# Optimization experiments

Hardware: AMD Instinct MI355X
Metric: run time of the kernel (lower is better)

Reference implementation:

```python
import jax, jax.numpy as jnp
import numpy as np

DIM = 512
LEVELS = 4
KSIZES = [3, 5, 7, 9]
NUM_HEADS = 4
GN_GROUPS = 4
GN_EPS = 1e-5
ROPE_BASE = 10000.0


def dwconv(x, w, b):
    # x: (B,C,H,W), w: (C,1,k,k) depthwise, b: (C,)
    y = jax.lax.conv_general_dilated(
        x, w, window_strides=(1, 1), padding='SAME',
        dimension_numbers=('NCHW', 'OIHW', 'NCHW'),
        feature_group_count=x.shape[1])
    return y + b[None, :, None, None]


def groupnorm(x, w, b):
    B, C, H, W = x.shape
    xg = x.reshape(B, GN_GROUPS, C // GN_GROUPS, H, W)
    mu = xg.mean(axis=(2, 3, 4), keepdims=True)
    var = xg.var(axis=(2, 3, 4), keepdims=True)
    xn = ((xg - mu) * jax.lax.rsqrt(var + GN_EPS)).reshape(B, C, H, W)
    return xn * w[None, :, None, None] + b[None, :, None, None]


def rope2d(x):
    # Faithful to the torch RoPE: rotations have shape (h, c//2) and broadcast
    # onto the trailing (w, c//2) dims of x (valid because h == w), so the
    # rotation angle effectively varies along the w axis.
    b, h, w, c = x.shape
    k_max = c // 2
    theta = 1.0 / (ROPE_BASE ** (jnp.arange(k_max, dtype=x.dtype) / k_max))
    angles = jnp.arange(h, dtype=x.dtype)[:, None] * theta[None, :]  # (h, k_max)
    cos = jnp.cos(angles)[None, None, :, :]  # broadcasts along w axis
    sin = jnp.sin(angles)[None, None, :, :]
    xp = x.reshape(b, h, w, k_max, 2)
    re, im = xp[..., 0], xp[..., 1]
    out_re = cos * re - sin * im
    out_im = cos * im + sin * re
    return jnp.stack([out_re, out_im], axis=-1).reshape(b, h, w, c)


def setup_inputs() -> dict:
    key = jax.random.key(0)
    ks = jax.random.split(key, 20)
    C = DIM
    inp = {'x': jax.random.normal(ks[0], (8, C, 64, 64), dtype=jnp.float32)}
    for i, k in enumerate(KSIZES):
        inp[f'conv_w{i}'] = jax.random.normal(ks[1 + i], (C, 1, k, k), dtype=jnp.float32) * 0.05
        inp[f'conv_b{i}'] = jnp.zeros((C,), dtype=jnp.float32)
        inp[f'gn_w{i}'] = jnp.ones((C,), dtype=jnp.float32)
        inp[f'gn_b{i}'] = jnp.zeros((C,), dtype=jnp.float32)
    inp['qk_w'] = jax.random.normal(ks[10], (2 * C, C), dtype=jnp.float32) * (C ** -0.5)
    inp['lepe_w'] = jax.random.normal(ks[11], (C, 1, 3, 3), dtype=jnp.float32) * 0.05
    inp['lepe_b'] = jnp.zeros((C,), dtype=jnp.float32)
    return inp


def reference(x, conv_w0, conv_b0, gn_w0, gn_b0, conv_w1, conv_b1, gn_w1, gn_b1,
              conv_w2, conv_b2, gn_w2, gn_b2, conv_w3, conv_b3, gn_w3, gn_b3,
              qk_w, lepe_w, lepe_b):
    conv_ws = [conv_w0, conv_w1, conv_w2, conv_w3]
    conv_bs = [conv_b0, conv_b1, conv_b2, conv_b3]
    gn_ws = [gn_w0, gn_w1, gn_w2, gn_w3]
    gn_bs = [gn_b0, gn_b1, gn_b2, gn_b3]

    # Multi-level depthwise conv -> GroupNorm -> sigmoid gate, averaged.
    fused = sum(jax.nn.sigmoid(groupnorm(dwconv(x, cw, cb), gw, gb))
                for cw, cb, gw, gb in zip(conv_ws, conv_bs, gn_ws, gn_bs)) / LEVELS

    b, c, h, w = fused.shape
    n = h * w
    H = NUM_HEADS
    hd = c // H

    tokens = fused.transpose(0, 2, 3, 1).reshape(b, n, c)  # (b, n, c)

    qk = tokens @ qk_w.T  # (b, n, 2c)
    q = jax.nn.elu(qk[..., :c]) + 1.0
    k = jax.nn.elu(qk[..., c:]) + 1.0
    v = tokens

    q_rope = rope2d(q.reshape(b, h, w, c)).reshape(b, n, H, hd).transpose(0, 2, 1, 3)
    k_rope = rope2d(k.reshape(b, h, w, c)).reshape(b, n, H, hd).transpose(0, 2, 1, 3)
    qh = q.reshape(b, n, H, hd).transpose(0, 2, 1, 3)  # (b,H,n,hd)
    kh = k.reshape(b, n, H, hd).transpose(0, 2, 1, 3)
    vh = v.reshape(b, n, H, hd).transpose(0, 2, 1, 3)

    k_mean = kh.mean(axis=2, keepdims=True)  # (b,H,1,hd)
    z = 1.0 / (jnp.einsum('bhnd,bhmd->bhnm', qh, k_mean) + 1e-6)  # (b,H,n,1)
    kv = jnp.einsum('bhnd,bhne->bhde', k_rope, vh) / n  # (b,H,hd,hd)
    attn = jnp.einsum('bhnd,bhde->bhne', q_rope, kv) * z  # (b,H,n,hd)

    out_tok = attn.transpose(0, 2, 1, 3).reshape(b, n, c)
    lepe_out = dwconv(fused, lepe_w, lepe_b)  # (b,c,h,w)
    out_tok = out_tok + lepe_out.transpose(0, 2, 3, 1).reshape(b, n, c)

    return out_tok.transpose(0, 2, 1).reshape(b, c, h, w)
```

## Files before the change

### kernel.cpp

```cpp
#include <hip/hip_runtime.h>
#include <math.h>


typedef __attribute__((ext_vector_type(8))) short bf8;
typedef __attribute__((ext_vector_type(4))) float f32x4;

__device__ __forceinline__ float waveSum(float v) {
  #pragma unroll
  for (int o = 32; o; o >>= 1) v += __shfl_down(v, o, 64);
  return v;
}

__device__ __forceinline__ unsigned short f2bf(float f) {
  unsigned u = __float_as_uint(f);
  unsigned r = u + 0x7fffu + ((u >> 16) & 1u);
  return (unsigned short)(r >> 16);
}

__device__ __forceinline__ float bf2f(unsigned short u) {
  return __uint_as_float((unsigned)u << 16);
}

__device__ __forceinline__ void gload_lds16(const void* g, void* l) {
  __builtin_amdgcn_global_load_lds(
      (const __attribute__((address_space(1))) unsigned*)g,
      (__attribute__((address_space(3))) unsigned*)l, 16, 0, 0);
}

__global__ __launch_bounds__(256) void k_ropetab(float* __restrict__ tab) {
  int idx = blockIdx.x * 256 + threadIdx.x;
  int w = idx >> 8, kk = idx & 255;
  float theta = powf(10000.0f, -(float)kk * (1.0f / 256.0f));
  float ang = (float)w * theta;
  tab[2 * idx]     = cosf(ang);
  tab[2 * idx + 1] = sinf(ang);
}

template <int K>
__device__ __forceinline__ void conv8(const float (*sm)[76], const float* wl,
                                      int r, int cb, float bias, float acc[8]) {
  constexpr int P = (K - 1) / 2;
  #pragma unroll
  for (int i = 0; i < 8; i++) acc[i] = bias;
  #pragma unroll
  for (int dy = 0; dy < K; ++dy) {
    const float* row = &sm[r + dy - P + 4][cb];
    float v[16];
    #pragma unroll
    for (int o = 0; o < 16; o += 4)
      *(float4*)&v[o] = *(const float4*)&row[o];
    #pragma unroll
    for (int dx = 0; dx < K; ++dx) {
      float wv = wl[dy * K + dx];
      #pragma unroll
      for (int i = 0; i < 8; i++)
        acc[i] = fmaf(wv, v[4 + i + dx - P], acc[i]);
    }
  }
}

__device__ __forceinline__ void load_plane512(const float* __restrict__ xp,
                                              float (*sm)[76], int tid) {
  for (int idx = tid; idx < 5184; idx += 512) {
    int pr = idx / 72, pc = idx - pr * 72;
    int gr = pr - 4, gc = pc - 4;
    float v = 0.f;
    if ((unsigned)gr < 64u && (unsigned)gc < 64u) v = xp[gr * 64 + gc];
    sm[pr][pc] = v;
  }
}

__device__ __forceinline__ void load_weights512(const float* w0, const float* w1,
                                                const float* w2, const float* w3,
                                                float* wl, int c, int tid) {
  if (tid < 9)               wl[tid] = w0[c * 9  + tid];
  else if (tid < 34)         wl[tid] = w1[c * 25 + tid - 9];
  else if (tid < 83)         wl[tid] = w2[c * 49 + tid - 34];
  else if (tid < 164)        wl[tid] = w3[c * 81 + tid - 83];
}

__device__ __forceinline__ void reduce_write2_512(float s, float sq, float* red,
                                                  int tid, float* dst) {
  s = waveSum(s); sq = waveSum(sq);
  int wid = tid >> 6, lane = tid & 63;
  if (lane == 0) { red[wid] = s; red[8 + wid] = sq; }
  __syncthreads();
  if (tid == 0) {
    float S = 0.f, SQ = 0.f;
    #pragma unroll
    for (int i = 0; i < 8; i++) { S += red[i]; SQ += red[8 + i]; }
    dst[0] = S; dst[1] = SQ;
  }
  __syncthreads();
}

__global__ __launch_bounds__(512) void k_conv4(
    const float* __restrict__ x,
    const float* __restrict__ w0, const float* __restrict__ b0,
    const float* __restrict__ w1, const float* __restrict__ b1,
    const float* __restrict__ w2, const float* __restrict__ b2,
    const float* __restrict__ w3, const float* __restrict__ b3,
    float* __restrict__ part,
    unsigned short* __restrict__ l0, unsigned short* __restrict__ l1,
    unsigned short* __restrict__ l2, unsigned short* __restrict__ l3) {
  __shared__ float sm[72][76];
  __shared__ float wl[164];
  __shared__ float red[16];
  int tid = threadIdx.x;
  int bc = blockIdx.x;
  int b = bc >> 9, c = bc & 511;
  load_plane512(x + (size_t)bc * 4096, sm, tid);
  load_weights512(w0, w1, w2, w3, wl, c, tid);
  __syncthreads();
  int r = tid >> 3, cb = (tid & 7) << 3;
  size_t obase = (size_t)bc * 4096 + r * 64 + cb;
  float acc[8];
  float s, sq;
  unsigned short o[8];

  conv8<3>(sm, &wl[0], r, cb, b0[c], acc);
  s = 0; sq = 0;
  #pragma unroll
  for (int i = 0; i < 8; i++) {
    s += acc[i]; sq = fmaf(acc[i], acc[i], sq); o[i] = f2bf(acc[i]);
  }
  *(uint4*)&l0[obase] = *(uint4*)&o[0];
  reduce_write2_512(s, sq, red, tid, part + ((size_t)(0 * 8 + b) * 512 + c) * 2);
  __builtin_amdgcn_sched_barrier(0);

  conv8<5>(sm, &wl[9], r, cb, b1[c], acc);
  s = 0; sq = 0;
  #pragma unroll
  for (int i = 0; i < 8; i++) {
    s += acc[i]; sq = fmaf(acc[i], acc[i], sq); o[i] = f2bf(acc[i]);
  }
  *(uint4*)&l1[obase] = *(uint4*)&o[0];
  reduce_write2_512(s, sq, red, tid, part + ((size_t)(1 * 8 + b) * 512 + c) * 2);
  __builtin_amdgcn_sched_barrier(0);

  conv8<7>(sm, &wl[34], r, cb, b2[c], acc);
  s = 0; sq = 0;
  #pragma unroll
  for (int i = 0; i < 8; i++) {
    s += acc[i]; sq = fmaf(acc[i], acc[i], sq); o[i] = f2bf(acc[i]);
  }
  *(uint4*)&l2[obase] = *(uint4*)&o[0];
  reduce_write2_512(s, sq, red, tid, part + ((size_t)(2 * 8 + b) * 512 + c) * 2);
  __builtin_amdgcn_sched_barrier(0);

  conv8<9>(sm, &wl[83], r, cb, b3[c], acc);
  s = 0; sq = 0;
  #pragma unroll
  for (int i = 0; i < 8; i++) {
    s += acc[i]; sq = fmaf(acc[i], acc[i], sq); o[i] = f2bf(acc[i]);
  }
  *(uint4*)&l3[obase] = *(uint4*)&o[0];
  reduce_write2_512(s, sq, red, tid, part + ((size_t)(3 * 8 + b) * 512 + c) * 2);
}

__global__ __launch_bounds__(128) void k_gn_stats(const float* __restrict__ part,
                                                  float* __restrict__ stats) {
  int blk = blockIdx.x;
  int tid = threadIdx.x;
  int g = blk & 3, bb = (blk >> 2) & 7, l = blk >> 5;
  const float* p = part + ((size_t)(l * 8 + bb) * 512 + g * 128 + tid) * 2;
  float s = p[0], sq = p[1];
  s = waveSum(s); sq = waveSum(sq);
  __shared__ float red[4];
  int wid = tid >> 6, lane = tid & 63;
  if (lane == 0) { red[wid] = s; red[2 + wid] = sq; }
  __syncthreads();
  if (tid == 0) {
    float S = red[0] + red[1], SQ = red[2] + red[3];
    const float inv = 1.0f / (128.0f * 4096.0f);
    float mean = S * inv;
    float var = SQ * inv - mean * mean;
    stats[blk * 2] = mean;
    stats[blk * 2 + 1] = rsqrtf(var + 1e-5f);
  }
}

__global__ __launch_bounds__(256) void k_fused_tp(
    const unsigned short* __restrict__ l0, const unsigned short* __restrict__ l1,
    const unsigned short* __restrict__ l2, const unsigned short* __restrict__ l3,
    const float* __restrict__ gw0, const float* __restrict__ gb0,
    const float* __restrict__ gw1, const float* __restrict__ gb1,
    const float* __restrict__ gw2, const float* __restrict__ gb2,
    const float* __restrict__ gw3, const float* __restrict__ gb3,
    const float* __restrict__ stats, float* __restrict__ fused,
    unsigned short* __restrict__ fbf) {
  __shared__ float smT[64][65];
  int tid = threadIdx.x;
  int bid = blockIdx.x;
  int nt = bid & 63, ct = (bid >> 6) & 7, b = bid >> 9;
  int c0 = ct << 6, n0 = nt << 6;
  int c_loc = tid >> 2, nq = tid & 3;
  int c = c0 + c_loc, g = c >> 7;
  float m0 = stats[(0 * 32 + b * 4 + g) * 2], r0 = stats[(0 * 32 + b * 4 + g) * 2 + 1];
  float m1 = stats[(1 * 32 + b * 4 + g) * 2], r1 = stats[(1 * 32 + b * 4 + g) * 2 + 1];
  float m2 = stats[(2 * 32 + b * 4 + g) * 2], r2 = stats[(2 * 32 + b * 4 + g) * 2 + 1];
  float m3 = stats[(3 * 32 + b * 4 + g) * 2], r3 = stats[(3 * 32 + b * 4 + g) * 2 + 1];
  float a0 = r0 * gw0[c], c0p = gb0[c] - m0 * a0;
  float a1 = r1 * gw1[c], c1p = gb1[c] - m1 * a1;
  float a2 = r2 * gw2[c], c2p = gb2[c] - m2 * a2;
  float a3 = r3 * gw3[c], c3p = gb3[c] - m3 * a3;
  size_t base = ((size_t)b * 512 + c) * 4096 + n0 + nq * 16;
  uint4 u0a = *(const uint4*)&l0[base], u0b = *(const uint4*)&l0[base + 8];
  uint4 u1a = *(const uint4*)&l1[base], u1b = *(const uint4*)&l1[base + 8];
  uint4 u2a = *(const uint4*)&l2[base], u2b = *(const uint4*)&l2[base + 8];
  uint4 u3a = *(const uint4*)&l3[base], u3b = *(const uint4*)&l3[base + 8];
  float outv[16];
  #pragma unroll
  for (int i = 0; i < 8; i++) {
    float t0 = fmaf(bf2f(((const unsigned short*)&u0a)[i]), a0, c0p);
    float t1 = fmaf(bf2f(((const unsigned short*)&u1a)[i]), a1, c1p);
    float t2 = fmaf(bf2f(((const unsigned short*)&u2a)[i]), a2, c2p);
    float t3 = fmaf(bf2f(((const unsigned short*)&u3a)[i]), a3, c3p);
    float s = 1.0f / (1.0f + __expf(-t0)) + 1.0f / (1.0f + __expf(-t1)) +
              1.0f / (1.0f + __expf(-t2)) + 1.0f / (1.0f + __expf(-t3));
    outv[i] = s * 0.25f;
  }
  #pragma unroll
  for (int i = 0; i < 8; i++) {
    float t0 = fmaf(bf2f(((const unsigned short*)&u0b)[i]), a0, c0p);
    float t1 = fmaf(bf2f(((const unsigned short*)&u1b)[i]), a1, c1p);
    float t2 = fmaf(bf2f(((const unsigned short*)&u2b)[i]), a2, c2p);
    float t3 = fmaf(bf2f(((const unsigned short*)&u3b)[i]), a3, c3p);
    float s = 1.0f / (1.0f + __expf(-t0)) + 1.0f / (1.0f + __expf(-t1)) +
              1.0f / (1.0f + __expf(-t2)) + 1.0f / (1.0f + __expf(-t3));
    outv[8 + i] = s * 0.25f;
  }
  float* fp = fused + base;
  #pragma unroll
  for (int i = 0; i < 16; i += 4)
    *(float4*)&fp[i] = make_float4(outv[i], outv[i + 1], outv[i + 2], outv[i + 3]);
  #pragma unroll
  for (int i = 0; i < 16; i++) smT[c_loc][nq * 16 + i] = outv[i];
  __syncthreads();
  int cc = tid & 63, r_s = tid >> 6;
  #pragma unroll
  for (int rr = 0; rr < 64; rr += 4)
    fbf[((size_t)b * 4096 + n0 + rr + r_s) * 512 + c0 + cc] = f2bf(smT[cc][rr + r_s]);
}

__global__ __launch_bounds__(256) void k_wcvt(const float* __restrict__ qkw,
                                              unsigned short* __restrict__ wbf) {
  int gid = blockIdx.x * 256 + threadIdx.x;
  float4 v = *(const float4*)&qkw[(size_t)gid * 4];
  short4 o;
  o.x = (short)f2bf(v.x); o.y = (short)f2bf(v.y);
  o.z = (short)f2bf(v.z); o.w = (short)f2bf(v.w);
  *(short4*)&wbf[(size_t)gid * 4] = o;
}

__global__ __launch_bounds__(256) void k_qk(const unsigned short* __restrict__ fbf,
                                            const unsigned short* __restrict__ wbf,
                                            float* __restrict__ qbuf,
                                            float* __restrict__ kbuf) {
  __shared__ __align__(16) short As[8192];
  __shared__ __align__(16) short Bs[8192];
  int tid = threadIdx.x;
  int bid = blockIdx.x;
  int sw = (bid & 7) * 256 + (bid >> 3);
  int b = sw >> 8, rem = sw & 255;
  int mt_blk = rem >> 3, jt = rem & 7;
  int m0 = mt_blk << 7, j0 = jt << 7;
  int lane = tid & 63, wid = tid >> 6;
  int wm = (wid >> 1) * 64, wn = (wid & 1) * 64;
  int l15 = lane & 15, l4 = lane >> 4;

  const unsigned short* Ab = fbf + (size_t)b * 4096 * 512;
  f32x4 acc[4][4];
  #pragma unroll
  for (int i = 0; i < 4; i++)
    #pragma unroll
    for (int j = 0; j < 4; j++) acc[i][j] = (f32x4)0.f;

  int srow[4], sperm[4];
  #pragma unroll
  for (int i = 0; i < 4; i++) {
    int s = i * 256 + tid;
    srow[i] = s >> 3;
    sperm[i] = (s & 7) ^ (srow[i] & 7);
  }

  for (int t = 0; t < 8; ++t) {
    int c0 = t << 6;
    if (t) __syncthreads();
    #pragma unroll
    for (int i = 0; i < 4; i++) {
      int s = i * 256 + tid;
      gload_lds16(Ab + (size_t)(m0 + srow[i]) * 512 + c0 + sperm[i] * 8,
                  (char*)As + s * 16);
      gload_lds16(wbf + (size_t)(j0 + srow[i]) * 512 + c0 + sperm[i] * 8,
                  (char*)Bs + s * 16);
    }
    __syncthreads();
    #pragma unroll
    for (int ks = 0; ks < 2; ++ks) {
      bf8 af[4], bfr[4];
      #pragma unroll
      for (int mt = 0; mt < 4; mt++) {
        int row = wm + mt * 16 + l15;
        int g = ks * 4 + l4;
        af[mt] = *(const bf8*)((const char*)As + row * 128 + ((g ^ (row & 7)) << 4));
      }
      #pragma unroll
      for (int nt = 0; nt < 4; nt++) {
        int row = wn + nt * 16 + l15;
        int g = ks * 4 + l4;
        bfr[nt] = *(const bf8*)((const char*)Bs + row * 128 + ((g ^ (row & 7)) << 4));
      }
      #pragma unroll
      for (int mt = 0; mt < 4; mt++)
        #pragma unroll
        for (int nt = 0; nt < 4; nt++)
          acc[mt][nt] = __builtin_amdgcn_mfma_f32_16x16x32_bf16(
              af[mt], bfr[nt], acc[mt][nt], 0, 0, 0);
    }
  }

  float* dst; int jb;
  if (j0 < 512) { dst = qbuf; jb = j0; } else { dst = kbuf; jb = j0 - 512; }
  #pragma unroll
  for (int mt = 0; mt < 4; mt++) {
    #pragma unroll
    for (int nt = 0; nt < 4; nt++) {
      #pragma unroll
      for (int r = 0; r < 4; r++) {
        float v = acc[mt][nt][r];
        v = v > 0.f ? v + 1.f : __expf(v);
        int token = m0 + wm + mt * 16 + l4 * 4 + r;
        int chan = jb + wn + nt * 16 + l15;
        dst[((size_t)b * 4096 + token) * 512 + chan] = v;
      }
    }
  }
}

__global__ __launch_bounds__(256) void k_krT(const float* __restrict__ kbuf,
                                             const float* __restrict__ tab,
                                             unsigned short* __restrict__ krT,
                                             float* __restrict__ kmp) {
  __shared__ float sm[64][65];
  int tid = threadIdx.x;
  int bid = blockIdx.x;
  int nt = bid & 63, ct = (bid >> 6) & 7, b = bid >> 9;
  int c0 = ct << 6, n0 = nt << 6;
  int cc = tid & 63, n_s = tid >> 6;
  #pragma unroll
  for (int nn = 0; nn < 64; nn += 4)
    sm[cc][nn + n_s] = kbuf[((size_t)b * 4096 + n0 + nn + n_s) * 512 + c0 + cc];
  __syncthreads();
  int rc = tid >> 2, nq = tid & 3;
  int c = c0 + rc;
  int pairidx = c >> 1;
  int odd = c & 1;
  int partner = odd ? rc - 1 : rc + 1;
  unsigned short o[16];
  float colsum = 0.f;
  #pragma unroll
  for (int i = 0; i < 16; i++) {
    int nloc = nq * 16 + i;
    float2 cs = *(const float2*)&tab[2 * (nloc * 256 + pairidx)];
    float a = sm[rc][nloc], p = sm[partner][nloc];
    float r = odd ? fmaf(cs.x, a, cs.y * p) : fmaf(cs.x, a, -cs.y * p);
    o[i] = f2bf(r);
    colsum += a;
  }
  *(uint4*)&krT[((size_t)b * 512 + c) * 4096 + n0 + nq * 16]     = *(uint4*)&o[0];
  *(uint4*)&krT[((size_t)b * 512 + c) * 4096 + n0 + nq * 16 + 8] = *(uint4*)&o[8];
  colsum += __shfl_xor(colsum, 1, 64);
  colsum += __shfl_xor(colsum, 2, 64);
  if (nq == 0) kmp[((size_t)b * 64 + nt) * 512 + c] = colsum;
}

__global__ __launch_bounds__(512) void k_kmean_fin(const float* __restrict__ kmp,
                                                   float* __restrict__ kmean) {
  int b = blockIdx.x, c = threadIdx.x;
  float s = 0.f;
  for (int nt = 0; nt < 64; nt++) s += kmp[((size_t)b * 64 + nt) * 512 + c];
  kmean[b * 512 + c] = s * (1.0f / 4096.0f);
}

__global__ __launch_bounds__(256) void k_zrope(const float* __restrict__ qbuf,
                                               const float* __restrict__ kmean,
                                               const float* __restrict__ tab,
                                               float* __restrict__ zbuf,
                                               unsigned short* __restrict__ qr) {
  __shared__ float kml[512];
  int tid = threadIdx.x;
  int blk = blockIdx.x;
  int b = blk >> 10;
  kml[tid] = kmean[b * 512 + tid];
  kml[tid + 256] = kmean[b * 512 + 256 + tid];
  __syncthreads();
  int tok = blk * 4 + (tid >> 6);
  int pg = tid & 63;
  int n = tok & 4095;
  int wpos = n & 63;
  const float* qp = qbuf + (size_t)tok * 512 + pg * 8;
  const float* tp = tab + 2 * (wpos * 256 + pg * 4);
  float4 a  = *(const float4*)&qp[0];
  float4 b4 = *(const float4*)&qp[4];
  float4 t0 = *(const float4*)&tp[0];
  float4 t1 = *(const float4*)&tp[4];
  unsigned short o[8];
  o[0] = f2bf(t0.x * a.x - t0.y * a.y);
  o[1] = f2bf(t0.x * a.y + t0.y * a.x);
  o[2] = f2bf(t0.z * a.z - t0.w * a.w);
  o[3] = f2bf(t0.z * a.w + t0.w * a.z);
  o[4] = f2bf(t1.x * b4.x - t1.y * b4.y);
  o[5] = f2bf(t1.x * b4.y + t1.y * b4.x);
  o[6] = f2bf(t1.z * b4.z - t1.w * b4.w);
  o[7] = f2bf(t1.z * b4.w + t1.w * b4.z);
  *(uint4*)&qr[(size_t)tok * 512 + pg * 8] = *(uint4*)o;
  const float* km = &kml[pg * 8];
  float4 ka = *(const float4*)&km[0];
  float4 kb = *(const float4*)&km[4];
  float dot = a.x * ka.x + a.y * ka.y + a.z * ka.z + a.w * ka.w +
              b4.x * kb.x + b4.y * kb.y + b4.z * kb.z + b4.w * kb.w;
  dot += __shfl_xor(dot, 1, 64);
  dot += __shfl_xor(dot, 2, 64);
  dot += __shfl_xor(dot, 4, 64);
  dot += __shfl_xor(dot, 8, 64);
  if ((pg & 15) == 0) {
    int h = pg >> 4;
    zbuf[(size_t)(b * 4 + h) * 4096 + n] = 1.0f / (dot + 1e-6f);
  }
}

__global__ __launch_bounds__(256) void k_kv(const unsigned short* __restrict__ krT,
                                            const float* __restrict__ fused,
                                            float* __restrict__ kvpart) {
  __shared__ __align__(16) short As[8192];
  __shared__ __align__(16) short Bs[8192];
  int tid = threadIdx.x;
  int bid = blockIdx.x;
  int bh = bid >> 3, chunk = bid & 7;
  int b = bh >> 2, h = bh & 3;
  int n_base = chunk * 512;
  int lane = tid & 63, wid = tid >> 6;
  int wm = (wid >> 1) * 64, wn = (wid & 1) * 64;
  int l15 = lane & 15, l4 = lane >> 4;

  const unsigned short* Ab = krT + ((size_t)b * 512 + h * 128) * 4096;
  const float* Vb = fused + ((size_t)b * 512 + h * 128) * 4096;
  f32x4 acc[4][4];
  #pragma unroll
  for (int i = 0; i < 4; i++)
    #pragma unroll
    for (int j = 0; j < 4; j++) acc[i][j] = (f32x4)0.f;

  int srow[4], sperm[4];
  #pragma unroll
  for (int i = 0; i < 4; i++) {
    int s = i * 256 + tid;
    srow[i] = s >> 3;
    sperm[i] = (s & 7) ^ (srow[i] & 7);
  }

  for (int t = 0; t < 8; ++t) {
    int k0 = n_base + (t << 6);
    if (t) __syncthreads();
    #pragma unroll
    for (int i = 0; i < 4; i++) {
      int s = i * 256 + tid;
      gload_lds16(Ab + (size_t)srow[i] * 4096 + k0 + sperm[i] * 8,
                  (char*)As + s * 16);
      const float* vp = &Vb[(size_t)srow[i] * 4096 + k0 + (s & 7) * 8];
      float4 v0 = *(const float4*)&vp[0];
      float4 v1 = *(const float4*)&vp[4];
      unsigned short o[8];
      o[0] = f2bf(v0.x); o[1] = f2bf(v0.y); o[2] = f2bf(v0.z); o[3] = f2bf(v0.w);
      o[4] = f2bf(v1.x); o[5] = f2bf(v1.y); o[6] = f2bf(v1.z); o[7] = f2bf(v1.w);
      *(uint4*)((char*)Bs + srow[i] * 128 + (sperm[i] << 4)) = *(uint4*)o;
    }
    __syncthreads();
    #pragma unroll
    for (int ks = 0; ks < 2; ++ks) {
      bf8 af[4], bfr[4];
      #pragma unroll
      for (int mt = 0; mt < 4; mt++) {
        int row = wm + mt * 16 + l15;
        int g = ks * 4 + l4;
        af[mt] = *(const bf8*)((const char*)As + row * 128 + ((g ^ (row & 7)) << 4));
      }
      #pragma unroll
      for (int nt = 0; nt < 4; nt++) {
        int row = wn + nt * 16 + l15;
        int g = ks * 4 + l4;
        bfr[nt] = *(const bf8*)((const char*)Bs + row * 128 + ((g ^ (row & 7)) << 4));
      }
      #pragma unroll
      for (int mt = 0; mt < 4; mt++)
        #pragma unroll
        for (int nt = 0; nt < 4; nt++)
          acc[mt][nt] = __builtin_amdgcn_mfma_f32_16x16x32_bf16(
              af[mt], bfr[nt], acc[mt][nt], 0, 0, 0);
    }
  }

  float* dst = kvpart + (size_t)(bh * 8 + chunk) * 16384;
  #pragma unroll
  for (int mt = 0; mt < 4; mt++) {
    #pragma unroll
    for (int nt = 0; nt < 4; nt++) {
      #pragma unroll
      for (int r = 0; r < 4; r++) {
        int d = wm + mt * 16 + l4 * 4 + r;
        int e = wn + nt * 16 + l15;
        dst[d * 128 + e] = acc[mt][nt][r];
      }
    }
  }
}

__global__ __launch_bounds__(256) void k_kv_fin(const float* __restrict__ part,
                                                unsigned short* __restrict__ kvT) {
  int bh = blockIdx.x;
  int tid = threadIdx.x;
  for (int idx = tid; idx < 16384; idx += 256) {
    int e = idx >> 7, d = idx & 127;
    float s = 0;
    for (int ch = 0; ch < 8; ch++)
      s += part[(size_t)(bh * 8 + ch) * 16384 + d * 128 + e];
    kvT[(size_t)bh * 16384 + idx] = f2bf(s * (1.0f / 4096.0f));
  }
}

__global__ __launch_bounds__(256) void k_lepe(const float* __restrict__ fused,
                                              const float* __restrict__ lw,
                                              const float* __restrict__ lb,
                                              float* __restrict__ out) {
  __shared__ float sm[66][67];
  __shared__ float wl[9];
  int tid = threadIdx.x;
  int bc = blockIdx.x;
  int c = bc & 511;
  const float* fp = fused + (size_t)bc * 4096;
  for (int idx = tid; idx < 4356; idx += 256) {
    int pr = idx / 66, pc = idx - pr * 66;
    int gr = pr - 1, gc = pc - 1;
    float v = 0.f;
    if ((unsigned)gr < 64u && (unsigned)gc < 64u) v = fp[gr * 64 + gc];
    sm[pr][pc] = v;
  }
  if (tid < 9) wl[tid] = lw[c * 9 + tid];
  __syncthreads();
  int r = tid >> 2, cb = (tid & 3) << 4;
  float bias = lb[c];
  float accv[16];
  #pragma unroll
  for (int i = 0; i < 16; i++) accv[i] = bias;
  #pragma unroll
  for (int dy = 0; dy < 3; dy++) {
    const float* row = &sm[r + dy][cb];
    float v[18];
    #pragma unroll
    for (int o = 0; o < 18; ++o) v[o] = row[o];
    #pragma unroll
    for (int dx = 0; dx < 3; dx++) {
      float wv = wl[dy * 3 + dx];
      #pragma unroll
      for (int i = 0; i < 16; i++) accv[i] = fmaf(wv, v[i + dx], accv[i]);
    }
  }
  float* op = out + (size_t)bc * 4096 + r * 64 + cb;
  #pragma unroll
  for (int i = 0; i < 16; i += 4)
    *(float4*)&op[i] = make_float4(accv[i], accv[i + 1], accv[i + 2], accv[i + 3]);
}

__global__ __launch_bounds__(256) void k_attn(const unsigned short* __restrict__ qr,
                                              const unsigned short* __restrict__ kvT,
                                              const float* __restrict__ zbuf,
                                              float* __restrict__ out) {
  __shared__ __align__(16) short As[8192];
  __shared__ __align__(16) short Bs[8192];
  __shared__ float zl[128];
  int tid = threadIdx.x;
  int bid = blockIdx.x;
  int sw = (bid & 7) * 128 + (bid >> 3);
  int b = sw >> 7, rem = sw & 127;
  int h = rem >> 5, mt_blk = rem & 31;
  int bh = b * 4 + h;
  int m0 = mt_blk << 7;
  int lane = tid & 63, wid = tid >> 6;
  int wm = (wid >> 1) * 64, wn = (wid & 1) * 64;
  int l15 = lane & 15, l4 = lane >> 4;

  const unsigned short* Ab = qr + (size_t)b * 4096 * 512 + h * 128;
  const unsigned short* Bb = kvT + (size_t)bh * 16384;
  if (tid < 128) zl[tid] = zbuf[(size_t)bh * 4096 + m0 + tid];

  f32x4 acc[4][4];
  #pragma unroll
  for (int i = 0; i < 4; i++)
    #pragma unroll
    for (int j = 0; j < 4; j++) acc[i][j] = (f32x4)0.f;

  int srow[4], sperm[4];
  #pragma unroll
  for (int i = 0; i < 4; i++) {
    int s = i * 256 + tid;
    srow[i] = s >> 3;
    sperm[i] = (s & 7) ^ (srow[i] & 7);
  }

  for (int t = 0; t < 2; ++t) {
    int c0 = t << 6;
    if (t) __syncthreads();
    #pragma unroll
    for (int i = 0; i < 4; i++) {
      int s = i * 256 + tid;
      gload_lds16(Ab + (size_t)(m0 + srow[i]) * 512 + c0 + sperm[i] * 8,
                  (char*)As + s * 16);
      gload_lds16(Bb + srow[i] * 128 + c0 + sperm[i] * 8,
                  (char*)Bs + s * 16);
    }
    __syncthreads();
    #pragma unroll
    for (int ks = 0; ks < 2; ++ks) {
      bf8 af[4], bfr[4];
      #pragma unroll
      for (int mt = 0; mt < 4; mt++) {
        int row = wm + mt * 16 + l15;
        int g = ks * 4 + l4;
        af[mt] = *(const bf8*)((const char*)As + row * 128 + ((g ^ (row & 7)) << 4));
      }
      #pragma unroll
      for (int nt = 0; nt < 4; nt++) {
        int row = wn + nt * 16 + l15;
        int g = ks * 4 + l4;
        bfr[nt] = *(const bf8*)((const char*)Bs + row * 128 + ((g ^ (row & 7)) << 4));
      }
      #pragma unroll
      for (int mt = 0; mt < 4; mt++)
        #pragma unroll
        for (int nt = 0; nt < 4; nt++)
          acc[mt][nt] = __builtin_amdgcn_mfma_f32_16x16x32_bf16(
              af[mt], bfr[nt], acc[mt][nt], 0, 0, 0);
    }
  }

  #pragma unroll
  for (int mt = 0; mt < 4; mt++) {
    int tl = wm + mt * 16 + l4 * 4;
    float4 zv = make_float4(zl[tl], zl[tl + 1], zl[tl + 2], zl[tl + 3]);
    #pragma unroll
    for (int nt = 0; nt < 4; nt++) {
      int e = wn + nt * 16 + l15;
      float* op = &out[((size_t)b * 512 + h * 128 + e) * 4096 + m0 + tl];
      float4 o4 = *(float4*)op;
      o4.x += acc[mt][nt][0] * zv.x;
      o4.y += acc[mt][nt][1] * zv.y;
      o4.z += acc[mt][nt][2] * zv.z;
      o4.w += acc[mt][nt][3] * zv.w;
      *(float4*)op = o4;
    }
  }
}

extern "C" void kernel_launch(void* const* d_in, const int* in_sizes, int n_in,
                              void* d_out, int out_size, void* d_ws, size_t ws_size,
                              hipStream_t stream) {
  (void)in_sizes; (void)n_in; (void)out_size; (void)ws_size;
  const float* x   = (const float*)d_in[0];
  const float* cw0 = (const float*)d_in[1];
  const float* cb0 = (const float*)d_in[2];
  const float* gw0 = (const float*)d_in[3];
  const float* gb0 = (const float*)d_in[4];
  const float* cw1 = (const float*)d_in[5];
  const float* cb1 = (const float*)d_in[6];
  const float* gw1 = (const float*)d_in[7];
  const float* gb1 = (const float*)d_in[8];
  const float* cw2 = (const float*)d_in[9];
  const float* cb2 = (const float*)d_in[10];
  const float* gw2 = (const float*)d_in[11];
  const float* gb2 = (const float*)d_in[12];
  const float* cw3 = (const float*)d_in[13];
  const float* cb3 = (const float*)d_in[14];
  const float* gw3 = (const float*)d_in[15];
  const float* gb3 = (const float*)d_in[16];
  const float* qkw = (const float*)d_in[17];
  const float* lw  = (const float*)d_in[18];
  const float* lb  = (const float*)d_in[19];
  float* out = (float*)d_out;
  float* ws  = (float*)d_ws;

  float* fused    = ws;
  float* qbuf     = fused + 16777216;
  float* convpart = qbuf + 16777216;
  float* gnstats  = convpart + 32768;
  float* tab      = gnstats + 256;
  float* kmp      = tab + 32768;
  float* kmean    = kmp + 262144;
  float* zbuf     = kmean + 4096;
  float* wslot    = zbuf + 131072;
  float* regionR  = wslot + 262144;
  float* kvpart   = regionR + 8388608;
  float* kbuf     = out;
  unsigned short* lvl0    = (unsigned short*)qbuf;
  unsigned short* lvl1    = (unsigned short*)kvpart;
  unsigned short* lvl2    = (unsigned short*)out;
  unsigned short* lvl3    = (unsigned short*)out + 16777216;
  unsigned short* fbf     = (unsigned short*)regionR;
  unsigned short* krT     = (unsigned short*)regionR;
  unsigned short* wbf     = (unsigned short*)wslot;
  unsigned short* kvT     = (unsigned short*)wslot;
  unsigned short* qropebf = (unsigned short*)fused;

  k_ropetab<<<dim3(64), dim3(256), 0, stream>>>(tab);
  k_conv4<<<dim3(4096), dim3(512), 0, stream>>>(
      x, cw0, cb0, cw1, cb1, cw2, cb2, cw3, cb3, convpart,
      lvl0, lvl1, lvl2, lvl3);
  k_gn_stats<<<dim3(128), dim3(128), 0, stream>>>(convpart, gnstats);
  k_fused_tp<<<dim3(4096), dim3(256), 0, stream>>>(
      lvl0, lvl1, lvl2, lvl3,
      gw0, gb0, gw1, gb1, gw2, gb2, gw3, gb3, gnstats, fused, fbf);
  k_wcvt<<<dim3(512), dim3(256), 0, stream>>>(qkw, wbf);
  k_qk<<<dim3(2048), dim3(256), 0, stream>>>(fbf, wbf, qbuf, kbuf);
  k_krT<<<dim3(4096), dim3(256), 0, stream>>>(kbuf, tab, krT, kmp);
  k_kmean_fin<<<dim3(8), dim3(512), 0, stream>>>(kmp, kmean);
  k_kv<<<dim3(256), dim3(256), 0, stream>>>(krT, fused, kvpart);
  k_kv_fin<<<dim3(32), dim3(256), 0, stream>>>(kvpart, kvT);
  k_lepe<<<dim3(4096), dim3(256), 0, stream>>>(fused, lw, lb, out);
  k_zrope<<<dim3(8192), dim3(256), 0, stream>>>(qbuf, kmean, tab, zbuf, qropebf);
  k_attn<<<dim3(1024), dim3(256), 0, stream>>>(qropebf, kvT, zbuf, out);
}
```

Baseline: 534.6 us.

## Store fused NCHW tensor as bf16 and pad conv LDS rows to 73

The fused tensor in NCHW layout is now written as bf16 instead of fp32. This halves its write traffic in k_fused_tp and its read traffic in k_kv and k_lepe. k_kv can now load V straight into LDS with global_load_lds instead of converting in registers. Separately, the conv shared-memory row pitch changes from 76 to 73 with scalar loads, aimed at LDS bank conflicts. The trade-offs are lost float4 LDS loads in the conv and bf16 rounding of the lepe input.

```diff
diff --git a/kernel.cpp b/kernel.cpp
--- a/kernel.cpp
+++ b/kernel.cpp
@@ -37,30 +37,28 @@
 }
 
 template <int K>
-__device__ __forceinline__ void conv8(const float (*sm)[76], const float* wl,
+__device__ __forceinline__ void conv8(float (*sm)[73], const float* wl,
                                       int r, int cb, float bias, float acc[8]) {
   constexpr int P = (K - 1) / 2;
   #pragma unroll
   for (int i = 0; i < 8; i++) acc[i] = bias;
   #pragma unroll
   for (int dy = 0; dy < K; ++dy) {
-    const float* row = &sm[r + dy - P + 4][cb];
-    float v[16];
-    #pragma unroll
-    for (int o = 0; o < 16; o += 4)
-      *(float4*)&v[o] = *(const float4*)&row[o];
+    const float* row = &sm[r + dy - P + 4][cb - P + 4];
+    float v[8 + K - 1];
+    #pragma unroll
+    for (int o = 0; o < 8 + K - 1; ++o) v[o] = row[o];
     #pragma unroll
     for (int dx = 0; dx < K; ++dx) {
       float wv = wl[dy * K + dx];
       #pragma unroll
-      for (int i = 0; i < 8; i++)
-        acc[i] = fmaf(wv, v[4 + i + dx - P], acc[i]);
+      for (int i = 0; i < 8; i++) acc[i] = fmaf(wv, v[i + dx], acc[i]);
     }
   }
 }
 
 __device__ __forceinline__ void load_plane512(const float* __restrict__ xp,
-                                              float (*sm)[76], int tid) {
+                                              float (*sm)[73], int tid) {
   for (int idx = tid; idx < 5184; idx += 512) {
     int pr = idx / 72, pc = idx - pr * 72;
     int gr = pr - 4, gc = pc - 4;
@@ -103,7 +101,7 @@
     float* __restrict__ part,
     unsigned short* __restrict__ l0, unsigned short* __restrict__ l1,
     unsigned short* __restrict__ l2, unsigned short* __restrict__ l3) {
-  __shared__ float sm[72][76];
+  __shared__ float sm[72][73];
   __shared__ float wl[164];
   __shared__ float red[16];
   int tid = threadIdx.x;
@@ -187,7 +185,7 @@
     const float* __restrict__ gw1, const float* __restrict__ gb1,
     const float* __restrict__ gw2, const float* __restrict__ gb2,
     const float* __restrict__ gw3, const float* __restrict__ gb3,
-    const float* __restrict__ stats, float* __restrict__ fused,
+    const float* __restrict__ stats, unsigned short* __restrict__ fnchw,
     unsigned short* __restrict__ fbf) {
   __shared__ float smT[64][65];
   int tid = threadIdx.x;
@@ -230,10 +228,11 @@
               1.0f / (1.0f + __expf(-t2)) + 1.0f / (1.0f + __expf(-t3));
     outv[8 + i] = s * 0.25f;
   }
-  float* fp = fused + base;
-  #pragma unroll
-  for (int i = 0; i < 16; i += 4)
-    *(float4*)&fp[i] = make_float4(outv[i], outv[i + 1], outv[i + 2], outv[i + 3]);
+  unsigned short ob[16];
+  #pragma unroll
+  for (int i = 0; i < 16; i++) ob[i] = f2bf(outv[i]);
+  *(uint4*)&fnchw[base]     = *(uint4*)&ob[0];
+  *(uint4*)&fnchw[base + 8] = *(uint4*)&ob[8];
   #pragma unroll
   for (int i = 0; i < 16; i++) smT[c_loc][nq * 16 + i] = outv[i];
   __syncthreads();
@@ -431,7 +430,7 @@
 }
 
 __global__ __launch_bounds__(256) void k_kv(const unsigned short* __restrict__ krT,
-                                            const float* __restrict__ fused,
+                                            const unsigned short* __restrict__ fnchw,
                                             float* __restrict__ kvpart) {
   __shared__ __align__(16) short As[8192];
   __shared__ __align__(16) short Bs[8192];
@@ -445,7 +444,7 @@
   int l15 = lane & 15, l4 = lane >> 4;
 
   const unsigned short* Ab = krT + ((size_t)b * 512 + h * 128) * 4096;
-  const float* Vb = fused + ((size_t)b * 512 + h * 128) * 4096;
+  const unsigned short* Vb = fnchw + ((size_t)b * 512 + h * 128) * 4096;
   f32x4 acc[4][4];
   #pragma unroll
   for (int i = 0; i < 4; i++)
@@ -468,13 +467,8 @@
       int s = i * 256 + tid;
       gload_lds16(Ab + (size_t)srow[i] * 4096 + k0 + sperm[i] * 8,
                   (char*)As + s * 16);
-      const float* vp = &Vb[(size_t)srow[i] * 4096 + k0 + (s & 7) * 8];
-      float4 v0 = *(const float4*)&vp[0];
-      float4 v1 = *(const float4*)&vp[4];
-      unsigned short o[8];
-      o[0] = f2bf(v0.x); o[1] = f2bf(v0.y); o[2] = f2bf(v0.z); o[3] = f2bf(v0.w);
-      o[4] = f2bf(v1.x); o[5] = f2bf(v1.y); o[6] = f2bf(v1.z); o[7] = f2bf(v1.w);
-      *(uint4*)((char*)Bs + srow[i] * 128 + (sperm[i] << 4)) = *(uint4*)o;
+      gload_lds16(Vb + (size_t)srow[i] * 4096 + k0 + sperm[i] * 8,
+                  (char*)Bs + s * 16);
     }
     __syncthreads();
     #pragma unroll
@@ -529,7 +523,7 @@
   }
 }
 
-__global__ __launch_bounds__(256) void k_lepe(const float* __restrict__ fused,
+__global__ __launch_bounds__(256) void k_lepe(const unsigned short* __restrict__ fnchw,
                                               const float* __restrict__ lw,
                                               const float* __restrict__ lb,
                                               float* __restrict__ out) {
@@ -538,12 +532,12 @@
   int tid = threadIdx.x;
   int bc = blockIdx.x;
   int c = bc & 511;
-  const float* fp = fused + (size_t)bc * 4096;
+  const unsigned short* fp = fnchw + (size_t)bc * 4096;
   for (int idx = tid; idx < 4356; idx += 256) {
     int pr = idx / 66, pc = idx - pr * 66;
     int gr = pr - 1, gc = pc - 1;
     float v = 0.f;
-    if ((unsigned)gr < 64u && (unsigned)gc < 64u) v = fp[gr * 64 + gc];
+    if ((unsigned)gr < 64u && (unsigned)gc < 64u) v = bf2f(fp[gr * 64 + gc]);
     sm[pr][pc] = v;
   }
   if (tid < 9) wl[tid] = lw[c * 9 + tid];
@@ -689,8 +683,8 @@
   float* out = (float*)d_out;
   float* ws  = (float*)d_ws;
 
-  float* fused    = ws;
-  float* qbuf     = fused + 16777216;
+  float* fslot    = ws;
+  float* qbuf     = fslot + 16777216;
   float* convpart = qbuf + 16777216;
   float* gnstats  = convpart + 32768;
   float* tab      = gnstats + 256;
@@ -705,11 +699,12 @@
   unsigned short* lvl1    = (unsigned short*)kvpart;
   unsigned short* lvl2    = (unsigned short*)out;
   unsigned short* lvl3    = (unsigned short*)out + 16777216;
+  unsigned short* fnchw   = (unsigned short*)fslot;
+  unsigned short* qropebf = (unsigned short*)fslot + 16777216;
   unsigned short* fbf     = (unsigned short*)regionR;
   unsigned short* krT     = (unsigned short*)regionR;
   unsigned short* wbf     = (unsigned short*)wslot;
   unsigned short* kvT     = (unsigned short*)wslot;
-  unsigned short* qropebf = (unsigned short*)fused;
 
   k_ropetab<<<dim3(64), dim3(256), 0, stream>>>(tab);
   k_conv4<<<dim3(4096), dim3(512), 0, stream>>>(
@@ -718,14 +713,14 @@
   k_gn_stats<<<dim3(128), dim3(128), 0, stream>>>(convpart, gnstats);
   k_fused_tp<<<dim3(4096), dim3(256), 0, stream>>>(
       lvl0, lvl1, lvl2, lvl3,
-      gw0, gb0, gw1, gb1, gw2, gb2, gw3, gb3, gnstats, fused, fbf);
+      gw0, gb0, gw1, gb1, gw2, gb2, gw3, gb3, gnstats, fnchw, fbf);
   k_wcvt<<<dim3(512), dim3(256), 0, stream>>>(qkw, wbf);
   k_qk<<<dim3(2048), dim3(256), 0, stream>>>(fbf, wbf, qbuf, kbuf);
   k_krT<<<dim3(4096), dim3(256), 0, stream>>>(kbuf, tab, krT, kmp);
   k_kmean_fin<<<dim3(8), dim3(512), 0, stream>>>(kmp, kmean);
-  k_kv<<<dim3(256), dim3(256), 0, stream>>>(krT, fused, kvpart);
+  k_kv<<<dim3(256), dim3(256), 0, stream>>>(krT, fnchw, kvpart);
   k_kv_fin<<<dim3(32), dim3(256), 0, stream>>>(kvpart, kvT);
-  k_lepe<<<dim3(4096), dim3(256), 0, stream>>>(fused, lw, lb, out);
+  k_lepe<<<dim3(4096), dim3(256), 0, stream>>>(fnchw, lw, lb, out);
   k_zrope<<<dim3(8192), dim3(256), 0, stream>>>(qbuf, kmean, tab, zbuf, qropebf);
   k_attn<<<dim3(1024), dim3(256), 0, stream>>>(qropebf, kvT, zbuf, out);
 }
```

After: 483.7 us. 9.5% less time.
